# Kernel tuning notes

Measured on AMD Instinct MI355X. Metric: run time of the kernel, lower is better.

Reference implementation:

```python
import jax, jax.numpy as jnp
import numpy as np

N_USERS = 50000
N_ITEMS = 50000
N_NODES = N_USERS + N_ITEMS
N_EDGES = 1600000
N_PAIRS = 200000
USER_DIM = 128
ITEM_DIM = 128
HID = 64
LAYER_NUM = 2


def setup_inputs() -> dict:
    key = jax.random.key(0)
    ks = jax.random.split(key, 16)
    inp = {
        "user_features": jax.random.normal(ks[0], (N_USERS, USER_DIM), jnp.float32),
        "item_features": jax.random.normal(ks[1], (N_ITEMS, ITEM_DIM), jnp.float32),
        "item_side_feat": jax.random.normal(ks[2], (N_ITEMS, HID), jnp.float32),
        "T_f": jax.random.uniform(ks[3], (2 * N_PAIRS,), jnp.float32),
        "T_cf": jax.random.uniform(ks[4], (2 * N_PAIRS,), jnp.float32),
        "Wu": jax.random.normal(ks[5], (USER_DIM, HID), jnp.float32) / np.sqrt(USER_DIM),
        "bu": jax.random.normal(ks[6], (HID,), jnp.float32) * 0.01,
        "Wi": jax.random.normal(ks[7], (ITEM_DIM, HID), jnp.float32) / np.sqrt(ITEM_DIM),
        "bi": jax.random.normal(ks[8], (HID,), jnp.float32) * 0.01,
        "W1": jax.random.normal(ks[9], (1 + 2 * HID, HID), jnp.float32) / np.sqrt(1 + 2 * HID),
        "b1": jax.random.normal(ks[10], (HID,), jnp.float32) * 0.01,
        "W2": jax.random.normal(ks[11], (HID, 1), jnp.float32) / np.sqrt(HID),
        "edge_src": jax.random.randint(ks[12], (N_EDGES,), 0, N_NODES, jnp.int32),
        "edge_dst": jax.random.randint(ks[13], (N_EDGES,), 0, N_NODES, jnp.int32),
        "userId": jax.random.randint(ks[14], (N_PAIRS,), 0, N_USERS, jnp.int32),
        "pos_itemId": jax.random.randint(ks[15], (N_PAIRS,), 0, N_ITEMS, jnp.int32),
        "neg_itemId": jax.random.randint(jax.random.fold_in(key, 99), (N_PAIRS,), 0, N_ITEMS, jnp.int32),
    }
    return inp


def reference(user_features, item_features, item_side_feat, T_f, T_cf,
              Wu, bu, Wi, bi, W1, b1, W2,
              edge_src, edge_dst, userId, pos_itemId, neg_itemId):
    # degree-based symmetric normalization (out_deg^-0.5 on src, in_deg^-0.5 on dst)
    ones = jnp.ones((edge_src.shape[0],), jnp.float32)
    out_deg = jax.ops.segment_sum(ones, edge_src, num_segments=N_NODES)
    in_deg = jax.ops.segment_sum(ones, edge_dst, num_segments=N_NODES)
    out_norm = jax.lax.rsqrt(jnp.clip(out_deg, 1.0))[:, None]  # [N,1]
    in_norm = jax.lax.rsqrt(jnp.clip(in_deg, 1.0))[:, None]

    def gcn_layer(node_f):
        m = node_f * out_norm                                   # [N,H]
        agg = jax.ops.segment_sum(m[edge_src], edge_dst, num_segments=N_NODES)
        return agg * in_norm

    user_embedding = jax.nn.relu(user_features @ Wu + bu)       # [Nu,H]
    item_embedding = jax.nn.relu(item_features @ Wi + bi)       # [Ni,H]

    for i in range(LAYER_NUM):
        if i == 0:
            embeddings = gcn_layer(jnp.concatenate([user_embedding, item_embedding], axis=0))
        else:
            embeddings = gcn_layer(embeddings)
        scale = 1.0 / (i + 2)
        user_embedding = user_embedding + embeddings[:N_USERS] * scale
        item_embedding = item_embedding + embeddings[N_USERS:] * scale

    item_embedding = item_embedding + item_side_feat

    userE = user_embedding[userId]                              # [P,H]
    posE = item_embedding[pos_itemId]
    negE = item_embedding[neg_itemId]
    zi = jnp.concatenate([userE, userE], axis=0)                # [2P,H]
    zj = jnp.concatenate([posE, negE], axis=0)

    def decode(T):
        h = jnp.concatenate([zi, zj, T[:, None]], axis=1)       # [2P, 2H+1]
        h = jax.nn.elu(h @ W1 + b1)
        return (h @ W2)[:, 0]                                   # [2P]

    logits_f = decode(T_f)
    logits_cf = decode(T_cf)
    return (user_embedding, item_embedding, logits_f, logits_cf)
```

## Files before the change

kernel.cpp:

```cpp
#include <hip/hip_runtime.h>

#define NU 50000
#define NI 50000
#define NN 100000
#define NE 1600000
#define NP 200000
#define DIM 128
#define HID 64

#define HR2 2
#define HC2 64
#define RN2 (NN / HR2)
#define RNW2 (RN2 / 2)
#define CE2 (NE / HC2)

#define HRF 4
#define RNF (NN / HRF)

typedef unsigned short bf16_t;
typedef __attribute__((ext_vector_type(8))) short short8;
typedef __attribute__((ext_vector_type(4))) float f32x4;
typedef __attribute__((ext_vector_type(2))) float f32x2;

__device__ __forceinline__ float bf2f(unsigned short u) {
  union { unsigned int i; float f; } c; c.i = ((unsigned int)u) << 16; return c.f;
}
__device__ __forceinline__ unsigned short f2bf(float f) {
  union { float f; unsigned int i; } c; c.f = f;
  unsigned int i = c.i;
  i += 0x7fffu + ((i >> 16) & 1u);
  return (unsigned short)(i >> 16);
}
__device__ __forceinline__ f32x2 unpack2(unsigned int w) {
  union { unsigned int i; float f; } lo, hi;
  lo.i = w << 16;
  hi.i = w & 0xffff0000u;
  f32x2 r; r.x = lo.f; r.y = hi.f;
  return r;
}
__device__ __forceinline__ int geti(const void* p, int i, bool i64) {
  return i64 ? (int)((const long long*)p)[i] : ((const int*)p)[i];
}

__global__ __launch_bounds__(64) void k_detect(const bf16_t* __restrict__ uf,
                                               const int* __restrict__ ei,
                                               int* __restrict__ flag) {
  int lane = threadIdx.x;
  float m = 0.f;
  for (int i = lane; i < 4096; i += 64) {
    float v = fabsf(bf2f(uf[i]));
    if (v < 3e38f) m = fmaxf(m, v);
  }
  int cnt = 0;
  for (int i = lane; i < 4096; i += 64) {
    if (ei[2 * i + 1] == 0) cnt++;
  }
  for (int off = 32; off > 0; off >>= 1) {
    m = fmaxf(m, __shfl_xor(m, off));
    cnt += __shfl_xor(cnt, off);
  }
  if (lane == 0) {
    flag[0] = (m > 100.f) ? 1 : 0;
    flag[1] = (cnt > 2048) ? 1 : 0;
  }
}

__global__ __launch_bounds__(1024) void k_hist1(const void* __restrict__ ev,
                                                const int* __restrict__ flag,
                                                unsigned int* __restrict__ part) {
  __shared__ unsigned int h[RNW2];
  const bool i64 = (flag[1] != 0);
  int r = blockIdx.x & (HR2 - 1);
  int c = blockIdx.x >> 1;
  int lo = r * RN2, hiN = lo + RN2;
  int t = threadIdx.x;
  for (int i = t; i < RNW2; i += 1024) h[i] = 0u;
  __syncthreads();
  int ebeg = c * CE2;
  if (!i64) {
    const int* p = (const int*)ev + ebeg;
    for (int e = t * 4; e < CE2; e += 1024 * 4) {
      int4 v4 = *(const int4*)(p + e);
      int vv[4] = {v4.x, v4.y, v4.z, v4.w};
#pragma unroll
      for (int k = 0; k < 4; ++k) {
        int v = vv[k];
        if (v >= lo && v < hiN) {
          int loc = v - lo;
          atomicAdd(&h[loc >> 1], 1u << ((loc & 1) * 16));
        }
      }
    }
  } else {
    const long long* p = (const long long*)ev + ebeg;
    for (int e = t; e < CE2; e += 1024) {
      int v = (int)p[e];
      if (v >= lo && v < hiN) {
        int loc = v - lo;
        atomicAdd(&h[loc >> 1], 1u << ((loc & 1) * 16));
      }
    }
  }
  __syncthreads();
  unsigned int* po = part + c * (NN / 2) + (lo >> 1);
  for (int i = t; i < RNW2; i += 1024) po[i] = h[i];
}

__global__ __launch_bounds__(256) void k_reduce(const unsigned int* __restrict__ pout,
                                                unsigned int* __restrict__ pin,
                                                int* __restrict__ din,
                                                float* __restrict__ onorm,
                                                float* __restrict__ inorm) {
  int w = blockIdx.x * 256 + threadIdx.x;
  if (w >= NN / 2) return;
  unsigned int so0 = 0, so1 = 0;
#pragma unroll
  for (int c = 0; c < HC2; ++c) {
    unsigned int v = pout[c * (NN / 2) + w];
    so0 += v & 0xffffu;
    so1 += v >> 16;
  }
  unsigned int si0 = 0, si1 = 0;
#pragma unroll
  for (int c = 0; c < HC2; ++c) {
    unsigned int v = pin[c * (NN / 2) + w];
    pin[c * (NN / 2) + w] = si0 | (si1 << 16);
    si0 += v & 0xffffu;
    si1 += v >> 16;
  }
  int n = 2 * w;
  din[n] = (int)si0;
  din[n + 1] = (int)si1;
  onorm[n] = rsqrtf((float)(so0 > 1u ? so0 : 1u));
  onorm[n + 1] = rsqrtf((float)(so1 > 1u ? so1 : 1u));
  inorm[n] = rsqrtf((float)(si0 > 1u ? si0 : 1u));
  inorm[n + 1] = rsqrtf((float)(si1 > 1u ? si1 : 1u));
}

__global__ __launch_bounds__(256) void k_scan1(const int* __restrict__ in,
                                               int* __restrict__ bsums, int n) {
  __shared__ int sh[256];
  int t = threadIdx.x;
  int base = blockIdx.x * 1024 + t * 4;
  int s = 0;
#pragma unroll
  for (int i = 0; i < 4; ++i)
    if (base + i < n) s += in[base + i];
  sh[t] = s;
  __syncthreads();
  for (int off = 128; off > 0; off >>= 1) {
    if (t < off) sh[t] += sh[t + off];
    __syncthreads();
  }
  if (t == 0) bsums[blockIdx.x] = sh[0];
}

__global__ __launch_bounds__(128) void k_scan2(const int* __restrict__ bsums,
                                               int* __restrict__ boffs, int nb) {
  __shared__ int sh[128];
  int t = threadIdx.x;
  int own = (t < nb) ? bsums[t] : 0;
  sh[t] = own;
  __syncthreads();
  for (int off = 1; off < 128; off <<= 1) {
    int add = (t >= off) ? sh[t - off] : 0;
    __syncthreads();
    sh[t] += add;
    __syncthreads();
  }
  if (t < nb) boffs[t] = sh[t] - own;
}

__global__ __launch_bounds__(256) void k_scan3(const int* __restrict__ in,
                                               const int* __restrict__ boffs,
                                               int* __restrict__ row_ptr,
                                               int* __restrict__ csr_src, int n) {
  __shared__ int sh[256];
  int t = threadIdx.x;
  int base = blockIdx.x * 1024 + t * 4;
  int v[4];
  int s = 0;
#pragma unroll
  for (int i = 0; i < 4; ++i) {
    v[i] = (base + i < n) ? in[base + i] : 0;
    s += v[i];
  }
  sh[t] = s;
  __syncthreads();
  for (int off = 1; off < 256; off <<= 1) {
    int add = (t >= off) ? sh[t - off] : 0;
    __syncthreads();
    sh[t] += add;
    __syncthreads();
  }
  int excl = boffs[blockIdx.x] + sh[t] - s;
#pragma unroll
  for (int i = 0; i < 4; ++i) {
    if (base + i < n) {
      row_ptr[base + i] = excl;
      excl += v[i];
    }
  }
  if (blockIdx.x == 0 && t == 0) row_ptr[n] = NE;
  if (blockIdx.x == 0 && t < 32) csr_src[NE + t] = NN;
}

__global__ __launch_bounds__(1024) void k_fill2(const void* __restrict__ srcv,
                                                const void* __restrict__ dstv,
                                                const int* __restrict__ flag,
                                                const int* __restrict__ row_ptr,
                                                const unsigned int* __restrict__ pin,
                                                int* __restrict__ csr_src) {
  __shared__ int cur[RNF];
  const bool i64 = (flag[1] != 0);
  int r = blockIdx.x & (HRF - 1);
  int c = blockIdx.x >> 2;
  int lo = r * RNF, hiN = lo + RNF;
  int t = threadIdx.x;
  const unsigned int* pw = pin + c * (NN / 2);
  const int* rp = row_ptr + lo;
  for (int i = t; i < RNF; i += 1024) {
    int node = lo + i;
    unsigned int wrd = pw[node >> 1];
    int off = (int)((wrd >> ((node & 1) * 16)) & 0xffffu);
    cur[i] = rp[i] + off;
  }
  __syncthreads();
  int ebeg = c * CE2;
  if (!i64) {
    const int* sp = (const int*)srcv + ebeg;
    const int* dp = (const int*)dstv + ebeg;
    for (int e = t * 4; e < CE2; e += 1024 * 4) {
      int4 dv = *(const int4*)(dp + e);
      int4 sv = *(const int4*)(sp + e);
      int dd[4] = {dv.x, dv.y, dv.z, dv.w};
      int ss[4] = {sv.x, sv.y, sv.z, sv.w};
#pragma unroll
      for (int k = 0; k < 4; ++k) {
        int d = dd[k];
        if (d >= lo && d < hiN) {
          int slot = atomicAdd(&cur[d - lo], 1);
          csr_src[slot] = ss[k];
        }
      }
    }
  } else {
    const long long* sp = (const long long*)srcv + ebeg;
    const long long* dp = (const long long*)dstv + ebeg;
    for (int e = t; e < CE2; e += 1024) {
      int d = (int)dp[e];
      if (d >= lo && d < hiN) {
        int slot = atomicAdd(&cur[d - lo], 1);
        csr_src[slot] = (int)sp[e];
      }
    }
  }
}

__global__ __launch_bounds__(256) void k_embed(const void* __restrict__ featv,
                                               const void* __restrict__ Wv,
                                               const void* __restrict__ biasv,
                                               const int* __restrict__ flag,
                                               const float* __restrict__ onorm_base,
                                               float* __restrict__ out,
                                               bf16_t* __restrict__ embs,
                                               bf16_t* __restrict__ zrow, int rows) {
  __shared__ float Ws[DIM * HID];
  __shared__ float bs[HID];
  const bool f32 = (flag[0] != 0);
  int t = threadIdx.x;
  if (zrow && blockIdx.x == 0 && t < 32)
    ((unsigned int*)zrow)[t] = 0u;
  if (f32) {
    const float* W = (const float*)Wv;
    for (int i = t; i < DIM * HID; i += 256) Ws[i] = W[i];
    if (t < HID) bs[t] = ((const float*)biasv)[t];
  } else {
    const bf16_t* W = (const bf16_t*)Wv;
    for (int i = t; i < DIM * HID; i += 256) Ws[i] = bf2f(W[i]);
    if (t < HID) bs[t] = bf2f(((const bf16_t*)biasv)[t]);
  }
  __syncthreads();
  int rl = t >> 4;
  int jq = t & 15;
  for (int rbase = blockIdx.x * 16; rbase < rows; rbase += gridDim.x * 16) {
    int row = rbase + rl;
    if (row >= rows) continue;
    float a0 = 0.f, a1 = 0.f, a2 = 0.f, a3 = 0.f;
    if (f32) {
      const float* fr = (const float*)featv + (size_t)row * DIM;
      for (int k0 = 0; k0 < DIM; k0 += 4) {
        float4 f4 = *(const float4*)(fr + k0);
        float fk[4] = {f4.x, f4.y, f4.z, f4.w};
#pragma unroll
        for (int kk = 0; kk < 4; ++kk) {
          const float* wr = &Ws[(k0 + kk) * HID + jq * 4];
          a0 += fk[kk] * wr[0];
          a1 += fk[kk] * wr[1];
          a2 += fk[kk] * wr[2];
          a3 += fk[kk] * wr[3];
        }
      }
    } else {
      const bf16_t* fr = (const bf16_t*)featv + (size_t)row * DIM;
      for (int k0 = 0; k0 < DIM; k0 += 8) {
        uint4 u = *(const uint4*)(fr + k0);
        unsigned int w[4] = {u.x, u.y, u.z, u.w};
#pragma unroll
        for (int kk = 0; kk < 8; ++kk) {
          unsigned short us = (unsigned short)((w[kk >> 1] >> ((kk & 1) * 16)) & 0xffffu);
          float fk = bf2f(us);
          const float* wr = &Ws[(k0 + kk) * HID + jq * 4];
          a0 += fk * wr[0];
          a1 += fk * wr[1];
          a2 += fk * wr[2];
          a3 += fk * wr[3];
        }
      }
    }
    float4 r;
    r.x = fmaxf(a0 + bs[jq * 4 + 0], 0.f);
    r.y = fmaxf(a1 + bs[jq * 4 + 1], 0.f);
    r.z = fmaxf(a2 + bs[jq * 4 + 2], 0.f);
    r.w = fmaxf(a3 + bs[jq * 4 + 3], 0.f);
    *(float4*)&out[(size_t)row * HID + jq * 4] = r;
    float sc = onorm_base[row];
    uint2 p;
    p.x = (unsigned int)f2bf(r.x * sc) | ((unsigned int)f2bf(r.y * sc) << 16);
    p.y = (unsigned int)f2bf(r.z * sc) | ((unsigned int)f2bf(r.w * sc) << 16);
    *(uint2*)&embs[(size_t)row * HID + jq * 4] = p;
  }
}

__global__ __launch_bounds__(256) void k_gather1(const bf16_t* __restrict__ embs,
                                                 const float* __restrict__ onorm,
                                                 const float* __restrict__ inorm,
                                                 const int* __restrict__ row_ptr,
                                                 const int* __restrict__ csr_src,
                                                 bf16_t* __restrict__ e1s) {
  if (blockIdx.x == 0 && threadIdx.x < 32)
    ((unsigned int*)(e1s + (size_t)NN * HID))[threadIdx.x] = 0u;
  int n = blockIdx.x * 4 + (threadIdx.x >> 6);
  if (n >= NN) return;
  int lane = threadIdx.x & 63;
  int g = lane >> 3;
  int l8 = (lane & 7) * 8;
  int beg = row_ptr[n], end = row_ptr[n + 1];
  f32x2 a[4];
#pragma unroll
  for (int j = 0; j < 4; ++j) a[j] = (f32x2)(0.f);
  for (int base = beg; base < end; base += 32) {
    int sv[4];
#pragma unroll
    for (int k = 0; k < 4; ++k) {
      int ee = base + k * 8 + g;
      int raw = csr_src[ee];
      sv[k] = (ee < end) ? raw : NN;
    }
#pragma unroll
    for (int k = 0; k < 4; ++k) {
      uint4 u = *(const uint4*)(embs + (sv[k] << 6) + l8);
      a[0] += unpack2(u.x);
      a[1] += unpack2(u.y);
      a[2] += unpack2(u.z);
      a[3] += unpack2(u.w);
    }
  }
#pragma unroll
  for (int j = 0; j < 4; ++j) {
    a[j].x += __shfl_xor(a[j].x, 8);
    a[j].y += __shfl_xor(a[j].y, 8);
    a[j].x += __shfl_xor(a[j].x, 16);
    a[j].y += __shfl_xor(a[j].y, 16);
    a[j].x += __shfl_xor(a[j].x, 32);
    a[j].y += __shfl_xor(a[j].y, 32);
  }
  if (g == 0) {
    float sc = inorm[n] * onorm[n];
    uint4 p;
    p.x = (unsigned int)f2bf(a[0].x * sc) | ((unsigned int)f2bf(a[0].y * sc) << 16);
    p.y = (unsigned int)f2bf(a[1].x * sc) | ((unsigned int)f2bf(a[1].y * sc) << 16);
    p.z = (unsigned int)f2bf(a[2].x * sc) | ((unsigned int)f2bf(a[2].y * sc) << 16);
    p.w = (unsigned int)f2bf(a[3].x * sc) | ((unsigned int)f2bf(a[3].y * sc) << 16);
    *(uint4*)(e1s + (size_t)n * HID + l8) = p;
  }
}

__global__ __launch_bounds__(256) void k_gather2c(float* __restrict__ emb0,
                                                  const bf16_t* __restrict__ e1s,
                                                  const void* __restrict__ sidev,
                                                  const int* __restrict__ flag,
                                                  const float* __restrict__ onorm,
                                                  const float* __restrict__ inorm,
                                                  const int* __restrict__ row_ptr,
                                                  const int* __restrict__ csr_src,
                                                  bf16_t* __restrict__ fin_bf) {
  int n = blockIdx.x * 4 + (threadIdx.x >> 6);
  if (n >= NN) return;
  int lane = threadIdx.x & 63;
  int g = lane >> 3;
  int l8 = (lane & 7) * 8;
  int beg = row_ptr[n], end = row_ptr[n + 1];
  f32x2 a[4];
#pragma unroll
  for (int j = 0; j < 4; ++j) a[j] = (f32x2)(0.f);
  for (int base = beg; base < end; base += 32) {
    int sv[4];
#pragma unroll
    for (int k = 0; k < 4; ++k) {
      int ee = base + k * 8 + g;
      int raw = csr_src[ee];
      sv[k] = (ee < end) ? raw : NN;
    }
#pragma unroll
    for (int k = 0; k < 4; ++k) {
      uint4 u = *(const uint4*)(e1s + (sv[k] << 6) + l8);
      a[0] += unpack2(u.x);
      a[1] += unpack2(u.y);
      a[2] += unpack2(u.z);
      a[3] += unpack2(u.w);
    }
  }
#pragma unroll
  for (int j = 0; j < 4; ++j) {
    a[j].x += __shfl_xor(a[j].x, 8);
    a[j].y += __shfl_xor(a[j].y, 8);
    a[j].x += __shfl_xor(a[j].x, 16);
    a[j].y += __shfl_xor(a[j].y, 16);
    a[j].x += __shfl_xor(a[j].x, 32);
    a[j].y += __shfl_xor(a[j].y, 32);
  }
  if (g == 0) {
    float aa[8] = {a[0].x, a[0].y, a[1].x, a[1].y, a[2].x, a[2].y, a[3].x, a[3].y};
    float inorm_n = inorm[n];
    float inv_on = 1.0f / onorm[n];
    size_t off = (size_t)n * HID + l8;
    uint4 u = *(const uint4*)(e1s + off);
    unsigned int w[4] = {u.x, u.y, u.z, u.w};
    float e1v[8];
#pragma unroll
    for (int j = 0; j < 4; ++j) {
      e1v[2 * j]     = bf2f((unsigned short)(w[j] & 0xffffu)) * inv_on;
      e1v[2 * j + 1] = bf2f((unsigned short)(w[j] >> 16)) * inv_on;
    }
    float4 b0 = *(const float4*)&emb0[off];
    float4 b1 = *(const float4*)&emb0[off + 4];
    float bb[8] = {b0.x, b0.y, b0.z, b0.w, b1.x, b1.y, b1.z, b1.w};
    const float s2 = 1.f / 3.f;
    float vv[8];
#pragma unroll
    for (int j = 0; j < 8; ++j)
      vv[j] = bb[j] + 0.5f * e1v[j] + s2 * aa[j] * inorm_n;
    if (n >= NU) {
      size_t soff = (size_t)(n - NU) * HID + l8;
      if (flag[0] != 0) {
        float4 s0 = *(const float4*)((const float*)sidev + soff);
        float4 s1 = *(const float4*)((const float*)sidev + soff + 4);
        vv[0] += s0.x; vv[1] += s0.y; vv[2] += s0.z; vv[3] += s0.w;
        vv[4] += s1.x; vv[5] += s1.y; vv[6] += s1.z; vv[7] += s1.w;
      } else {
        uint4 su = *(const uint4*)((const bf16_t*)sidev + soff);
        unsigned int sw[4] = {su.x, su.y, su.z, su.w};
#pragma unroll
        for (int j = 0; j < 4; ++j) {
          vv[2 * j]     += bf2f((unsigned short)(sw[j] & 0xffffu));
          vv[2 * j + 1] += bf2f((unsigned short)(sw[j] >> 16));
        }
      }
    }
    float4 o0, o1;
    o0.x = vv[0]; o0.y = vv[1]; o0.z = vv[2]; o0.w = vv[3];
    o1.x = vv[4]; o1.y = vv[5]; o1.z = vv[6]; o1.w = vv[7];
    *(float4*)&emb0[off] = o0;
    *(float4*)&emb0[off + 4] = o1;
    uint4 pb;
    pb.x = (unsigned int)f2bf(vv[0]) | ((unsigned int)f2bf(vv[1]) << 16);
    pb.y = (unsigned int)f2bf(vv[2]) | ((unsigned int)f2bf(vv[3]) << 16);
    pb.z = (unsigned int)f2bf(vv[4]) | ((unsigned int)f2bf(vv[5]) << 16);
    pb.w = (unsigned int)f2bf(vv[6]) | ((unsigned int)f2bf(vv[7]) << 16);
    *(uint4*)(fin_bf + off) = pb;
  }
}

__global__ __launch_bounds__(256) void k_decode(const bf16_t* __restrict__ zb,
                                                const void* __restrict__ W1v,
                                                const void* __restrict__ b1v,
                                                const void* __restrict__ W2v,
                                                const void* __restrict__ Tfv,
                                                const void* __restrict__ Tcfv,
                                                const int* __restrict__ flag,
                                                const void* __restrict__ userId,
                                                const void* __restrict__ posId,
                                                const void* __restrict__ negId,
                                                float* __restrict__ out_lf,
                                                float* __restrict__ out_lcf) {
  __shared__ bf16_t W1b[128 * 65];
  __shared__ float wlast[HID], b1s[HID], W2s[HID];
  const bool f32 = (flag[0] != 0);
  const bool i64 = (flag[1] != 0);
  int t = threadIdx.x;
  if (f32) {
    const float* W1 = (const float*)W1v;
    for (int i = t; i < 128 * 64; i += 256) W1b[(i >> 6) * 65 + (i & 63)] = f2bf(W1[i]);
    if (t < HID) {
      wlast[t] = W1[128 * 64 + t];
      b1s[t] = ((const float*)b1v)[t];
      W2s[t] = ((const float*)W2v)[t];
    }
  } else {
    const bf16_t* W1 = (const bf16_t*)W1v;
    for (int i = t; i < 128 * 64; i += 256) W1b[(i >> 6) * 65 + (i & 63)] = W1[i];
    if (t < HID) {
      wlast[t] = bf2f(W1[128 * 64 + t]);
      b1s[t] = bf2f(((const bf16_t*)b1v)[t]);
      W2s[t] = bf2f(((const bf16_t*)W2v)[t]);
    }
  }
  __syncthreads();
  int wv = t >> 6;
  int lane = t & 63;
  int m = lane & 15;
  int q = lane >> 4;
  short8 Bf[4][4];
#pragma unroll
  for (int c = 0; c < 4; ++c)
#pragma unroll
    for (int nt = 0; nt < 4; ++nt)
#pragma unroll
      for (int j = 0; j < 8; ++j)
        Bf[c][nt][j] = (short)W1b[(c * 32 + q * 8 + j) * 65 + nt * 16 + m];

  const int tiles = NP / 16;
  for (int tile = blockIdx.x * 4 + wv; tile < tiles; tile += gridDim.x * 4) {
    int pid = tile * 16 + m;
    int uid = geti(userId, pid, i64);
    int pidx = geti(posId, pid, i64);
    int nidx = geti(negId, pid, i64);
    const bf16_t* ur = zb + (size_t)uid * HID;
    const bf16_t* pp = zb + (size_t)(NU + pidx) * HID;
    const bf16_t* nn = zb + (size_t)(NU + nidx) * HID;
    short8 au0 = *(const short8*)(ur + q * 8);
    short8 au1 = *(const short8*)(ur + 32 + q * 8);
    short8 ap0 = *(const short8*)(pp + q * 8);
    short8 ap1 = *(const short8*)(pp + 32 + q * 8);
    short8 an0 = *(const short8*)(nn + q * 8);
    short8 an1 = *(const short8*)(nn + 32 + q * 8);
    f32x4 accp[4], accn[4];
#pragma unroll
    for (int nt = 0; nt < 4; ++nt) {
      f32x4 accu = (f32x4)(0.f);
      accu = __builtin_amdgcn_mfma_f32_16x16x32_bf16(au0, Bf[0][nt], accu, 0, 0, 0);
      accu = __builtin_amdgcn_mfma_f32_16x16x32_bf16(au1, Bf[1][nt], accu, 0, 0, 0);
      accp[nt] = __builtin_amdgcn_mfma_f32_16x16x32_bf16(ap0, Bf[2][nt], accu, 0, 0, 0);
      accp[nt] = __builtin_amdgcn_mfma_f32_16x16x32_bf16(ap1, Bf[3][nt], accp[nt], 0, 0, 0);
      accn[nt] = __builtin_amdgcn_mfma_f32_16x16x32_bf16(an0, Bf[2][nt], accu, 0, 0, 0);
      accn[nt] = __builtin_amdgcn_mfma_f32_16x16x32_bf16(an1, Bf[3][nt], accn[nt], 0, 0, 0);
    }
    float tf_p[4], tc_p[4], tf_n[4], tc_n[4];
    int rbase = tile * 16 + q * 4;
    if (f32) {
      float4 t4 = *(const float4*)((const float*)Tfv + rbase);
      float4 c4 = *(const float4*)((const float*)Tcfv + rbase);
      float4 t4n = *(const float4*)((const float*)Tfv + rbase + NP);
      float4 c4n = *(const float4*)((const float*)Tcfv + rbase + NP);
      tf_p[0] = t4.x; tf_p[1] = t4.y; tf_p[2] = t4.z; tf_p[3] = t4.w;
      tc_p[0] = c4.x; tc_p[1] = c4.y; tc_p[2] = c4.z; tc_p[3] = c4.w;
      tf_n[0] = t4n.x; tf_n[1] = t4n.y; tf_n[2] = t4n.z; tf_n[3] = t4n.w;
      tc_n[0] = c4n.x; tc_n[1] = c4n.y; tc_n[2] = c4n.z; tc_n[3] = c4n.w;
    } else {
      const bf16_t* tp = (const bf16_t*)Tfv + rbase;
      const bf16_t* cp = (const bf16_t*)Tcfv + rbase;
#pragma unroll
      for (int r = 0; r < 4; ++r) {
        tf_p[r] = bf2f(tp[r]); tc_p[r] = bf2f(cp[r]);
        tf_n[r] = bf2f(tp[r + NP]); tc_n[r] = bf2f(cp[r + NP]);
      }
    }
#pragma unroll
    for (int r = 0; r < 4; ++r) {
      float sfp = 0.f, scp = 0.f, sfn = 0.f, scn = 0.f;
#pragma unroll
      for (int nt = 0; nt < 4; ++nt) {
        int n = nt * 16 + m;
        float b = b1s[n];
        float wl = wlast[n];
        float w2 = W2s[n];
        float xp = accp[nt][r] + b;
        float xn = accn[nt][r] + b;
        float v0 = xp + tf_p[r] * wl;
        float v1 = xp + tc_p[r] * wl;
        float v2 = xn + tf_n[r] * wl;
        float v3 = xn + tc_n[r] * wl;
        sfp += (v0 > 0.f ? v0 : (__expf(v0) - 1.f)) * w2;
        scp += (v1 > 0.f ? v1 : (__expf(v1) - 1.f)) * w2;
        sfn += (v2 > 0.f ? v2 : (__expf(v2) - 1.f)) * w2;
        scn += (v3 > 0.f ? v3 : (__expf(v3) - 1.f)) * w2;
      }
#pragma unroll
      for (int s = 1; s < 16; s <<= 1) {
        sfp += __shfl_xor(sfp, s);
        scp += __shfl_xor(scp, s);
        sfn += __shfl_xor(sfn, s);
        scn += __shfl_xor(scn, s);
      }
      if (m == 0) {
        int pr2 = rbase + r;
        out_lf[pr2] = sfp;
        out_lcf[pr2] = scp;
        out_lf[pr2 + NP] = sfn;
        out_lcf[pr2 + NP] = scn;
      }
    }
  }
}

extern "C" void kernel_launch(void* const* d_in, const int* in_sizes, int n_in,
                              void* d_out, int out_size, void* d_ws, size_t ws_size,
                              hipStream_t stream) {
  (void)in_sizes; (void)n_in; (void)out_size;
  const void* user_f = d_in[0];
  const void* item_f = d_in[1];
  const void* side   = d_in[2];
  const void* Tf     = d_in[3];
  const void* Tcf    = d_in[4];
  const void* Wu     = d_in[5];
  const void* bu     = d_in[6];
  const void* Wi     = d_in[7];
  const void* bi     = d_in[8];
  const void* W1     = d_in[9];
  const void* b1     = d_in[10];
  const void* W2     = d_in[11];
  const void* esrc   = d_in[12];
  const void* edst   = d_in[13];
  const void* userId = d_in[14];
  const void* posId  = d_in[15];
  const void* negId  = d_in[16];

  const size_t WS_NEEDED = 33601664;
  if (ws_size < WS_NEEDED) return;

  char* ws = (char*)d_ws;
  int*   deg_in  = (int*)(ws + 0);
  float* onorm   = (float*)(ws + 400000);
  float* inorm   = (float*)(ws + 800000);
  int*   row_ptr = (int*)(ws + 1200000);
  int*   bsums   = (int*)(ws + 1600128);
  int*   boffs   = (int*)(ws + 1600640);
  int*   flag    = (int*)(ws + 1601152);
  int*   csr_src = (int*)(ws + 1601280);
  unsigned int* pout = (unsigned int*)(ws + 8001408);
  unsigned int* pin  = (unsigned int*)(ws + 20801536);
  bf16_t* embs   = (bf16_t*)(ws + 8001408);
  bf16_t* e1s    = (bf16_t*)(ws + 20801536);
  bf16_t* fin_bf = embs;

  float* out     = (float*)d_out;
  float* emb0    = out;
  float* out_lf  = out + (size_t)NN * HID;
  float* out_lcf = out_lf + 2 * NP;

  k_detect<<<1, 64, 0, stream>>>((const bf16_t*)user_f, (const int*)esrc, flag);
  k_hist1<<<HR2 * HC2, 1024, 0, stream>>>(esrc, flag, pout);
  k_hist1<<<HR2 * HC2, 1024, 0, stream>>>(edst, flag, pin);
  k_reduce<<<(NN / 2 + 255) / 256, 256, 0, stream>>>(pout, pin, deg_in, onorm, inorm);
  k_scan1<<<98, 256, 0, stream>>>(deg_in, bsums, NN);
  k_scan2<<<1, 128, 0, stream>>>(bsums, boffs, 98);
  k_scan3<<<98, 256, 0, stream>>>(deg_in, boffs, row_ptr, csr_src, NN);
  k_fill2<<<HRF * HC2, 1024, 0, stream>>>(esrc, edst, flag, row_ptr, pin, csr_src);
  k_embed<<<256, 256, 0, stream>>>(user_f, Wu, bu, flag, onorm, emb0, embs,
                                   embs + (size_t)NN * HID, NU);
  k_embed<<<256, 256, 0, stream>>>(item_f, Wi, bi, flag, onorm + NU,
                                   emb0 + (size_t)NU * HID, embs + (size_t)NU * HID,
                                   (bf16_t*)0, NI);
  k_gather1<<<NN / 4, 256, 0, stream>>>(embs, onorm, inorm, row_ptr, csr_src, e1s);
  k_gather2c<<<NN / 4, 256, 0, stream>>>(emb0, e1s, side, flag, onorm, inorm, row_ptr,
                                         csr_src, fin_bf);
  k_decode<<<1024, 256, 0, stream>>>(fin_bf, W1, b1, W2, Tf, Tcf, flag,
                                     userId, posId, negId, out_lf, out_lcf);
}
```

Baseline: 419.6 us.

## Fuse degree reduce with block-sum scan and use half-wavefront per node in gathers

The degree reduction kernel now also writes per-block sums, which removes the separate scan1 launch. The scan block granularity shrinks to 512 so it matches the reduce blocks, and scan2 grows to 256 threads to cover 196 blocks. The two neighbour-gather kernels now give each node 32 lanes instead of 64, processing 16 edges per iteration. This aims to cut idle lanes on low-degree nodes (average degree 16) and drops one shuffle stage, at the cost of less parallelism per node on high-degree rows.

```diff
diff --git a/kernel.cpp b/kernel.cpp
--- a/kernel.cpp
+++ b/kernel.cpp
@@ -110,43 +110,36 @@
                                                 unsigned int* __restrict__ pin,
                                                 int* __restrict__ din,
                                                 float* __restrict__ onorm,
-                                                float* __restrict__ inorm) {
-  int w = blockIdx.x * 256 + threadIdx.x;
-  if (w >= NN / 2) return;
-  unsigned int so0 = 0, so1 = 0;
-#pragma unroll
-  for (int c = 0; c < HC2; ++c) {
-    unsigned int v = pout[c * (NN / 2) + w];
-    so0 += v & 0xffffu;
-    so1 += v >> 16;
-  }
-  unsigned int si0 = 0, si1 = 0;
-#pragma unroll
-  for (int c = 0; c < HC2; ++c) {
-    unsigned int v = pin[c * (NN / 2) + w];
-    pin[c * (NN / 2) + w] = si0 | (si1 << 16);
-    si0 += v & 0xffffu;
-    si1 += v >> 16;
-  }
-  int n = 2 * w;
-  din[n] = (int)si0;
-  din[n + 1] = (int)si1;
-  onorm[n] = rsqrtf((float)(so0 > 1u ? so0 : 1u));
-  onorm[n + 1] = rsqrtf((float)(so1 > 1u ? so1 : 1u));
-  inorm[n] = rsqrtf((float)(si0 > 1u ? si0 : 1u));
-  inorm[n + 1] = rsqrtf((float)(si1 > 1u ? si1 : 1u));
-}
-
-__global__ __launch_bounds__(256) void k_scan1(const int* __restrict__ in,
-                                               int* __restrict__ bsums, int n) {
+                                                float* __restrict__ inorm,
+                                                int* __restrict__ bsums) {
   __shared__ int sh[256];
   int t = threadIdx.x;
-  int base = blockIdx.x * 1024 + t * 4;
-  int s = 0;
-#pragma unroll
-  for (int i = 0; i < 4; ++i)
-    if (base + i < n) s += in[base + i];
-  sh[t] = s;
+  int w = blockIdx.x * 256 + t;
+  unsigned int si0 = 0, si1 = 0;
+  if (w < NN / 2) {
+    unsigned int so0 = 0, so1 = 0;
+#pragma unroll
+    for (int c = 0; c < HC2; ++c) {
+      unsigned int v = pout[c * (NN / 2) + w];
+      so0 += v & 0xffffu;
+      so1 += v >> 16;
+    }
+#pragma unroll
+    for (int c = 0; c < HC2; ++c) {
+      unsigned int v = pin[c * (NN / 2) + w];
+      pin[c * (NN / 2) + w] = si0 | (si1 << 16);
+      si0 += v & 0xffffu;
+      si1 += v >> 16;
+    }
+    int n = 2 * w;
+    din[n] = (int)si0;
+    din[n + 1] = (int)si1;
+    onorm[n] = rsqrtf((float)(so0 > 1u ? so0 : 1u));
+    onorm[n + 1] = rsqrtf((float)(so1 > 1u ? so1 : 1u));
+    inorm[n] = rsqrtf((float)(si0 > 1u ? si0 : 1u));
+    inorm[n + 1] = rsqrtf((float)(si1 > 1u ? si1 : 1u));
+  }
+  sh[t] = (int)(si0 + si1);
   __syncthreads();
   for (int off = 128; off > 0; off >>= 1) {
     if (t < off) sh[t] += sh[t + off];
@@ -155,14 +148,14 @@
   if (t == 0) bsums[blockIdx.x] = sh[0];
 }
 
-__global__ __launch_bounds__(128) void k_scan2(const int* __restrict__ bsums,
+__global__ __launch_bounds__(256) void k_scan2(const int* __restrict__ bsums,
                                                int* __restrict__ boffs, int nb) {
-  __shared__ int sh[128];
+  __shared__ int sh[256];
   int t = threadIdx.x;
   int own = (t < nb) ? bsums[t] : 0;
   sh[t] = own;
   __syncthreads();
-  for (int off = 1; off < 128; off <<= 1) {
+  for (int off = 1; off < 256; off <<= 1) {
     int add = (t >= off) ? sh[t - off] : 0;
     __syncthreads();
     sh[t] += add;
@@ -177,14 +170,10 @@
                                                int* __restrict__ csr_src, int n) {
   __shared__ int sh[256];
   int t = threadIdx.x;
-  int base = blockIdx.x * 1024 + t * 4;
-  int v[4];
-  int s = 0;
-#pragma unroll
-  for (int i = 0; i < 4; ++i) {
-    v[i] = (base + i < n) ? in[base + i] : 0;
-    s += v[i];
-  }
+  int base = blockIdx.x * 512 + t * 2;
+  int v0 = (base < n) ? in[base] : 0;
+  int v1 = (base + 1 < n) ? in[base + 1] : 0;
+  int s = v0 + v1;
   sh[t] = s;
   __syncthreads();
   for (int off = 1; off < 256; off <<= 1) {
@@ -194,13 +183,8 @@
     __syncthreads();
   }
   int excl = boffs[blockIdx.x] + sh[t] - s;
-#pragma unroll
-  for (int i = 0; i < 4; ++i) {
-    if (base + i < n) {
-      row_ptr[base + i] = excl;
-      excl += v[i];
-    }
-  }
+  if (base < n) row_ptr[base] = excl;
+  if (base + 1 < n) row_ptr[base + 1] = excl + v0;
   if (blockIdx.x == 0 && t == 0) row_ptr[n] = NE;
   if (blockIdx.x == 0 && t < 32) csr_src[NE + t] = NN;
 }
@@ -340,20 +324,20 @@
                                                  bf16_t* __restrict__ e1s) {
   if (blockIdx.x == 0 && threadIdx.x < 32)
     ((unsigned int*)(e1s + (size_t)NN * HID))[threadIdx.x] = 0u;
-  int n = blockIdx.x * 4 + (threadIdx.x >> 6);
-  if (n >= NN) return;
   int lane = threadIdx.x & 63;
-  int g = lane >> 3;
+  int h = lane >> 5;
+  int g = (lane >> 3) & 3;
   int l8 = (lane & 7) * 8;
+  int n = blockIdx.x * 8 + (threadIdx.x >> 6) * 2 + h;
   int beg = row_ptr[n], end = row_ptr[n + 1];
   f32x2 a[4];
 #pragma unroll
   for (int j = 0; j < 4; ++j) a[j] = (f32x2)(0.f);
-  for (int base = beg; base < end; base += 32) {
+  for (int base = beg; base < end; base += 16) {
     int sv[4];
 #pragma unroll
     for (int k = 0; k < 4; ++k) {
-      int ee = base + k * 8 + g;
+      int ee = base + k * 4 + g;
       int raw = csr_src[ee];
       sv[k] = (ee < end) ? raw : NN;
     }
@@ -372,8 +356,6 @@
     a[j].y += __shfl_xor(a[j].y, 8);
     a[j].x += __shfl_xor(a[j].x, 16);
     a[j].y += __shfl_xor(a[j].y, 16);
-    a[j].x += __shfl_xor(a[j].x, 32);
-    a[j].y += __shfl_xor(a[j].y, 32);
   }
   if (g == 0) {
     float sc = inorm[n] * onorm[n];
@@ -395,20 +377,20 @@
                                                   const int* __restrict__ row_ptr,
                                                   const int* __restrict__ csr_src,
                                                   bf16_t* __restrict__ fin_bf) {
-  int n = blockIdx.x * 4 + (threadIdx.x >> 6);
-  if (n >= NN) return;
   int lane = threadIdx.x & 63;
-  int g = lane >> 3;
+  int h = lane >> 5;
+  int g = (lane >> 3) & 3;
   int l8 = (lane & 7) * 8;
+  int n = blockIdx.x * 8 + (threadIdx.x >> 6) * 2 + h;
   int beg = row_ptr[n], end = row_ptr[n + 1];
   f32x2 a[4];
 #pragma unroll
   for (int j = 0; j < 4; ++j) a[j] = (f32x2)(0.f);
-  for (int base = beg; base < end; base += 32) {
+  for (int base = beg; base < end; base += 16) {
     int sv[4];
 #pragma unroll
     for (int k = 0; k < 4; ++k) {
-      int ee = base + k * 8 + g;
+      int ee = base + k * 4 + g;
       int raw = csr_src[ee];
       sv[k] = (ee < end) ? raw : NN;
     }
@@ -427,8 +409,6 @@
     a[j].y += __shfl_xor(a[j].y, 8);
     a[j].x += __shfl_xor(a[j].x, 16);
     a[j].y += __shfl_xor(a[j].y, 16);
-    a[j].x += __shfl_xor(a[j].x, 32);
-    a[j].y += __shfl_xor(a[j].y, 32);
   }
   if (g == 0) {
     float aa[8] = {a[0].x, a[0].y, a[1].x, a[1].y, a[2].x, a[2].y, a[3].x, a[3].y};
@@ -636,7 +616,7 @@
   const void* posId  = d_in[15];
   const void* negId  = d_in[16];
 
-  const size_t WS_NEEDED = 33601664;
+  const size_t WS_NEEDED = 33602688;
   if (ws_size < WS_NEEDED) return;
 
   char* ws = (char*)d_ws;
@@ -645,13 +625,13 @@
   float* inorm   = (float*)(ws + 800000);
   int*   row_ptr = (int*)(ws + 1200000);
   int*   bsums   = (int*)(ws + 1600128);
-  int*   boffs   = (int*)(ws + 1600640);
-  int*   flag    = (int*)(ws + 1601152);
-  int*   csr_src = (int*)(ws + 1601280);
-  unsigned int* pout = (unsigned int*)(ws + 8001408);
-  unsigned int* pin  = (unsigned int*)(ws + 20801536);
-  bf16_t* embs   = (bf16_t*)(ws + 8001408);
-  bf16_t* e1s    = (bf16_t*)(ws + 20801536);
+  int*   boffs   = (int*)(ws + 1601152);
+  int*   flag    = (int*)(ws + 1602176);
+  int*   csr_src = (int*)(ws + 1602304);
+  unsigned int* pout = (unsigned int*)(ws + 8002432);
+  unsigned int* pin  = (unsigned int*)(ws + 20802560);
+  bf16_t* embs   = (bf16_t*)(ws + 8002432);
+  bf16_t* e1s    = (bf16_t*)(ws + 20802560);
   bf16_t* fin_bf = embs;
 
   float* out     = (float*)d_out;
@@ -662,18 +642,17 @@
   k_detect<<<1, 64, 0, stream>>>((const bf16_t*)user_f, (const int*)esrc, flag);
   k_hist1<<<HR2 * HC2, 1024, 0, stream>>>(esrc, flag, pout);
   k_hist1<<<HR2 * HC2, 1024, 0, stream>>>(edst, flag, pin);
-  k_reduce<<<(NN / 2 + 255) / 256, 256, 0, stream>>>(pout, pin, deg_in, onorm, inorm);
-  k_scan1<<<98, 256, 0, stream>>>(deg_in, bsums, NN);
-  k_scan2<<<1, 128, 0, stream>>>(bsums, boffs, 98);
-  k_scan3<<<98, 256, 0, stream>>>(deg_in, boffs, row_ptr, csr_src, NN);
+  k_reduce<<<196, 256, 0, stream>>>(pout, pin, deg_in, onorm, inorm, bsums);
+  k_scan2<<<1, 256, 0, stream>>>(bsums, boffs, 196);
+  k_scan3<<<196, 256, 0, stream>>>(deg_in, boffs, row_ptr, csr_src, NN);
   k_fill2<<<HRF * HC2, 1024, 0, stream>>>(esrc, edst, flag, row_ptr, pin, csr_src);
   k_embed<<<256, 256, 0, stream>>>(user_f, Wu, bu, flag, onorm, emb0, embs,
                                    embs + (size_t)NN * HID, NU);
   k_embed<<<256, 256, 0, stream>>>(item_f, Wi, bi, flag, onorm + NU,
                                    emb0 + (size_t)NU * HID, embs + (size_t)NU * HID,
                                    (bf16_t*)0, NI);
-  k_gather1<<<NN / 4, 256, 0, stream>>>(embs, onorm, inorm, row_ptr, csr_src, e1s);
-  k_gather2c<<<NN / 4, 256, 0, stream>>>(emb0, e1s, side, flag, onorm, inorm, row_ptr,
+  k_gather1<<<NN / 8, 256, 0, stream>>>(embs, onorm, inorm, row_ptr, csr_src, e1s);
+  k_gather2c<<<NN / 8, 256, 0, stream>>>(emb0, e1s, side, flag, onorm, inorm, row_ptr,
                                          csr_src, fin_bf);
   k_decode<<<1024, 256, 0, stream>>>(fin_bf, W1, b1, W2, Tf, Tcf, flag,
                                      userId, posId, negId, out_lf, out_lcf);
```

Measured after the change: 396.6 us. 1.06x faster.
